# Performance work log

Hardware: AMD Instinct MI355X
Metric: run time of the kernel (lower is better)

Reference implementation:

```python
import jax, jax.numpy as jnp
import numpy as np

N, T, INPUT_DIM, HIDDEN_DIM = 8, 4096, 128, 128


def setup_inputs() -> dict:
    key = jax.random.key(0)
    k_h, k_wq, k_bq, k_wk, k_bk = jax.random.split(key, 5)
    s = 1.0 / np.sqrt(INPUT_DIM)
    return {
        "H": jax.random.normal(k_h, (N, T, INPUT_DIM), dtype=jnp.float32),
        "Wq": jax.random.uniform(k_wq, (INPUT_DIM, HIDDEN_DIM), jnp.float32, -s, s),
        "bq": jax.random.uniform(k_bq, (HIDDEN_DIM,), jnp.float32, -s, s),
        "Wk": jax.random.uniform(k_wk, (INPUT_DIM, HIDDEN_DIM), jnp.float32, -s, s),
        "bk": jax.random.uniform(k_bk, (HIDDEN_DIM,), jnp.float32, -s, s),
    }


def reference(H, Wq, bq, Wk, bk):
    # Q, K: [N, T, hidden]
    Q = jnp.einsum("ntd,dh->nth", H, Wq) + bq
    K = jnp.einsum("ntd,dh->nth", H, Wk) + bk
    # Faithful quirk: original scales by sqrt(K.transpose(-1,-2).size(-1)) == sqrt(T),
    # NOT sqrt(hidden_dim).
    T_ = H.shape[1]
    scale = 1.0 / jnp.sqrt(jnp.asarray(T_, dtype=H.dtype))
    A = jnp.einsum("nth,nsh->nts", Q, K) * scale  # [N, T, T]
    A = jax.nn.softmax(A, axis=-1)
    # Attention applied directly to H (no V projection), plus residual.
    return jnp.einsum("nts,nsd->ntd", A, H) + H
```

## Files before the change

kernel.cpp:

```cpp
#include <hip/hip_runtime.h>
#include <hip/hip_bf16.h>

typedef __attribute__((ext_vector_type(4))) float f32x4;
typedef __attribute__((ext_vector_type(16))) float f32x16;
typedef __attribute__((ext_vector_type(8))) short s16x8;
typedef unsigned int u32;

#define DEVINL static __device__ __forceinline__

constexpr int TDIM = 4096;
constexpr int DDIM = 128;
constexpr float QSCALE = 1.4426950408889634f / 64.0f;

DEVINL unsigned short f2bf(float f) {
  union { float f; unsigned u; } v; v.f = f;
  unsigned r = v.u + 0x7fffu + ((v.u >> 16) & 1u);
  return (unsigned short)(r >> 16);
}

__global__ __launch_bounds__(256) void prep_kernel(
    const float* __restrict__ Wq, const float* __restrict__ Wk,
    const float* __restrict__ bq, unsigned short* __restrict__ Mt,
    float* __restrict__ u) {
  int idx = blockIdx.x * 256 + threadIdx.x;
  int e = idx >> 7, d = idx & 127;
  float acc = 0.f;
#pragma unroll 4
  for (int h = 0; h < 128; ++h) acc += Wq[d * 128 + h] * Wk[e * 128 + h];
  Mt[e * 128 + d] = f2bf(acc);
  if (blockIdx.x == 0 && threadIdx.x < 128) {
    float a = 0.f;
#pragma unroll 4
    for (int h = 0; h < 128; ++h) a += Wk[threadIdx.x * 128 + h] * bq[h];
    u[threadIdx.x] = a;
  }
}

__global__ __launch_bounds__(256) void proj_kernel(
    const float* __restrict__ H, const unsigned short* __restrict__ Mt,
    const float* __restrict__ u, char* __restrict__ Qb,
    char* __restrict__ Kb, char* __restrict__ Vt) {
  __shared__ __align__(16) unsigned short hs[64][136];
  __shared__ __align__(16) char qs[16384];
  __shared__ __align__(16) char kt[16384];
  __shared__ __align__(16) char vt[16384];
  int b = blockIdx.x;
  int n = b >> 6;
  int t0 = (b & 63) << 6;
  int tid = threadIdx.x;
  const float* Hrow = H + (size_t)(n * TDIM + t0) * DDIM;
#pragma unroll
  for (int k = 0; k < 8; ++k) {
    int e = tid + k * 256;
    int r = e >> 5;
    int c = (e & 31) << 2;
    f32x4 v = *(const f32x4*)(Hrow + r * DDIM + c);
    unsigned short bf[4] = {f2bf(v.x), f2bf(v.y), f2bf(v.z), f2bf(v.w)};
    unsigned short* p = &hs[r][c];
    p[0] = bf[0]; p[1] = bf[1]; p[2] = bf[2]; p[3] = bf[3];
    int kbyte = r * 256 + ((c * 2) ^ ((r & 15) << 4));
    unsigned short* kp = (unsigned short*)(kt + kbyte);
    kp[0] = bf[0]; kp[1] = bf[1]; kp[2] = bf[2]; kp[3] = bf[3];
    int p32 = r >> 5, tl = r & 31;
#pragma unroll
    for (int j = 0; j < 4; ++j) {
      int d = c + j;
      int dp = d >> 1, half = d & 1;
      int byte = p32 * 8192 + dp * 128 +
                 ((half * 64 + tl * 2) ^ ((dp & 7) << 4));
      *(unsigned short*)(vt + byte) = bf[j];
    }
  }
  __syncthreads();
  int w = tid >> 6, ln = tid & 63;
  int lm = ln & 15, lg = ln >> 4;
  int m0 = w * 16;
  s16x8 af[4];
#pragma unroll
  for (int kf = 0; kf < 4; ++kf)
    af[kf] = *(const s16x8*)&hs[m0 + lm][kf * 32 + lg * 8];
#pragma unroll
  for (int nt = 0; nt < 8; ++nt) {
    f32x4 acc = {0.f, 0.f, 0.f, 0.f};
#pragma unroll
    for (int kf = 0; kf < 4; ++kf) {
      s16x8 bfr = *(const s16x8*)&Mt[(nt * 16 + lm) * 128 + kf * 32 + lg * 8];
      acc = __builtin_amdgcn_mfma_f32_16x16x32_bf16(af[kf], bfr, acc, 0, 0, 0);
    }
    int e = nt * 16 + lm;
    float bv = u[e];
#pragma unroll
    for (int i = 0; i < 4; ++i) {
      int tl = m0 + lg * 4 + i;
      int byte = tl * 256 + ((e * 2) ^ ((tl & 15) << 4));
      *(unsigned short*)(qs + byte) = f2bf((acc[i] + bv) * QSCALE);
    }
  }
  __syncthreads();
  size_t base = (size_t)(n * TDIM + t0) * 256;
  size_t vbase = (size_t)(n * 128 + (t0 >> 5)) * 8192;
#pragma unroll
  for (int k = 0; k < 4; ++k) {
    int off = tid * 16 + k * 4096;
    *(f32x4*)(Qb + base + off) = *(const f32x4*)(qs + off);
    *(f32x4*)(Kb + base + off) = *(const f32x4*)(kt + off);
    *(f32x4*)(Vt + vbase + off) = *(const f32x4*)(vt + off);
  }
}

DEVINL void stage8(const char* g, char* s, int ln) {
#pragma unroll
  for (int j = 0; j < 8; ++j) {
    __builtin_amdgcn_global_load_lds(
        (const __attribute__((address_space(1))) void*)(g + j * 1024 + ln * 16),
        (__attribute__((address_space(3))) void*)(s + j * 1024), 16, 0, 0);
  }
}

__global__ __launch_bounds__(512, 2) void attn_kernel(
    const char* __restrict__ Qsw, const char* __restrict__ Ksw,
    const char* __restrict__ Vsw, const float* __restrict__ H,
    float* __restrict__ Out) {
  __shared__ __align__(16) char lds[131072];
  int b = blockIdx.x;
  int n = b & 7;
  int q0 = (b >> 3) << 7;
  int tid = threadIdx.x;
  int w = tid >> 6, ln = tid & 63;
  int q32 = ln & 31, hi = ln >> 5;
  int qg = w >> 2;
  int kvs = w & 3;
  int qrow = q0 + qg * 64;
  int swz = (q32 & 15) << 4;
  int dpl = q32 >> 1;
  int vcol = (q32 & 1) * 64;

  const char* Kn = Ksw + (size_t)n * (TDIM * 256);
  const char* Vn = Vsw + (size_t)n * (128 * 8192);

  const char* Qlo = Qsw + (size_t)(n * TDIM + qrow + q32) * 256;
  const char* Qhi = Qlo + 32 * 256;
  s16x8 qfl[8], qfh[8];
#pragma unroll
  for (int d = 0; d < 8; ++d) {
    int off = (d * 32 + hi * 16) ^ swz;
    qfl[d] = *(const s16x8*)(Qlo + off);
    qfh[d] = *(const s16x8*)(Qhi + off);
  }

  f32x16 o[8];
#pragma unroll
  for (int i = 0; i < 8; ++i) o[i] = (f32x16)0.0f;
  float lsl = 0.f, lsh = 0.f;

  int stp = w & 3, typ = w >> 2;
  {
    const char* g = typ ? (Vn + (size_t)(stp * 32) * 8192)
                        : (Kn + (size_t)(stp * 1024) * 256);
    stage8(g, lds + stp * 16384 + typ * 8192, ln);
  }
  __syncthreads();

  for (int it = 0; it < 32; ++it) {
    int c = it & 1;
    if (it < 31) {
      int kvn = stp * 1024 + (it + 1) * 32;
      const char* g = typ ? (Vn + (size_t)(kvn >> 5) * 8192)
                          : (Kn + (size_t)kvn * 256);
      stage8(g, lds + (c ^ 1) * 65536 + stp * 16384 + typ * 8192, ln);
    }
    const char* kb = lds + c * 65536 + kvs * 16384;
    const char* vb = kb + 8192;

    f32x16 sl = (f32x16)0.0f, sh = (f32x16)0.0f;
    __builtin_amdgcn_s_setprio(1);
#pragma unroll
    for (int d = 0; d < 8; ++d) {
      s16x8 ka = *(const s16x8*)(kb + (q32 * 256 + ((d * 32 + hi * 16) ^ swz)));
      sl = __builtin_amdgcn_mfma_f32_32x32x16_bf16(ka, qfl[d], sl, 0, 0, 0);
      sh = __builtin_amdgcn_mfma_f32_32x32x16_bf16(ka, qfh[d], sh, 0, 0, 0);
    }
    __builtin_amdgcn_s_setprio(0);

#pragma unroll
    for (int r = 0; r < 16; ++r) {
      sl[r] = __builtin_amdgcn_exp2f(sl[r]);
      lsl += sl[r];
      sh[r] = __builtin_amdgcn_exp2f(sh[r]);
      lsh += sh[r];
    }

    s16x8 pal[2], pah[2];
    {
      u32 P2[8];
#pragma unroll
      for (int r = 0; r < 8; ++r)
        asm("v_cvt_pk_bf16_f32 %0, %1, %2"
            : "=v"(P2[r]) : "v"(sl[2 * r]), "v"(sl[2 * r + 1]));
#pragma unroll
      for (int b2 = 0; b2 < 2; ++b2) {
        u32 a0 = P2[b2 * 4 + 0], c0 = P2[b2 * 4 + 2];
        u32 a1 = P2[b2 * 4 + 1], c1 = P2[b2 * 4 + 3];
        asm("v_permlane32_swap_b32 %0, %1" : "+v"(a0), "+v"(c0));
        asm("v_permlane32_swap_b32 %0, %1" : "+v"(a1), "+v"(c1));
        union { u32 u[4]; s16x8 v; } pk;
        pk.u[0] = a0; pk.u[1] = a1; pk.u[2] = c0; pk.u[3] = c1;
        pal[b2] = pk.v;
      }
#pragma unroll
      for (int r = 0; r < 8; ++r)
        asm("v_cvt_pk_bf16_f32 %0, %1, %2"
            : "=v"(P2[r]) : "v"(sh[2 * r]), "v"(sh[2 * r + 1]));
#pragma unroll
      for (int b2 = 0; b2 < 2; ++b2) {
        u32 a0 = P2[b2 * 4 + 0], c0 = P2[b2 * 4 + 2];
        u32 a1 = P2[b2 * 4 + 1], c1 = P2[b2 * 4 + 3];
        asm("v_permlane32_swap_b32 %0, %1" : "+v"(a0), "+v"(c0));
        asm("v_permlane32_swap_b32 %0, %1" : "+v"(a1), "+v"(c1));
        union { u32 u[4]; s16x8 v; } pk;
        pk.u[0] = a0; pk.u[1] = a1; pk.u[2] = c0; pk.u[3] = c1;
        pah[b2] = pk.v;
      }
    }

    __builtin_amdgcn_s_setprio(1);
#pragma unroll
    for (int ks = 0; ks < 2; ++ks) {
#pragma unroll
      for (int dt = 0; dt < 4; ++dt) {
        s16x8 vv = *(const s16x8*)(vb + ((dt * 16 + dpl) * 128 +
                        ((vcol + ks * 32 + hi * 16) ^ ((dpl & 7) << 4))));
        o[dt] = __builtin_amdgcn_mfma_f32_32x32x16_bf16(pal[ks], vv, o[dt], 0, 0, 0);
        o[4 + dt] = __builtin_amdgcn_mfma_f32_32x32x16_bf16(pah[ks], vv, o[4 + dt], 0, 0, 0);
      }
    }
    __builtin_amdgcn_s_setprio(0);
    __syncthreads();
  }

#define DUMP_O(dst)                                                      \
  {                                                                      \
    char* _d = (dst);                                                    \
    _Pragma("unroll") for (int i = 0; i < 8; ++i)                        \
      _Pragma("unroll") for (int c4 = 0; c4 < 4; ++c4) {                 \
        f32x4 ch = {o[i][c4 * 4 + 0], o[i][c4 * 4 + 1],                  \
                    o[i][c4 * 4 + 2], o[i][c4 * 4 + 3]};                 \
        *(f32x4*)(_d + ((i * 4 + c4) * 64 + ln) * 16) = ch;              \
      }                                                                  \
  }
#define ADD_O(src)                                                       \
  {                                                                      \
    const char* _s = (src);                                              \
    _Pragma("unroll") for (int i = 0; i < 8; ++i)                        \
      _Pragma("unroll") for (int c4 = 0; c4 < 4; ++c4) {                 \
        f32x4 ch = *(const f32x4*)(_s + ((i * 4 + c4) * 64 + ln) * 16);  \
        o[i][c4 * 4 + 0] += ch.x; o[i][c4 * 4 + 1] += ch.y;              \
        o[i][c4 * 4 + 2] += ch.z; o[i][c4 * 4 + 3] += ch.w;              \
      }                                                                  \
  }
  if (kvs & 1) DUMP_O(lds + (qg * 2 + (kvs >> 1)) * 32768);
  __syncthreads();
  if (!(kvs & 1)) ADD_O(lds + (qg * 2 + (kvs >> 1)) * 32768);
  __syncthreads();
  if (kvs == 2) DUMP_O(lds + qg * 2 * 32768);
  {
    float* lt = (float*)(lds + (qg * 2 + 1) * 32768);
    lt[((kvs * 2 + hi) * 32 + q32) * 2 + 0] = lsl;
    lt[((kvs * 2 + hi) * 32 + q32) * 2 + 1] = lsh;
  }
  __syncthreads();
  if (kvs == 0) {
    ADD_O(lds + qg * 2 * 32768);
    const float* lt = (const float*)(lds + (qg * 2 + 1) * 32768);
    const float* Hn = H + (size_t)n * TDIM * DDIM;
    float* On = Out + (size_t)n * TDIM * DDIM;
#pragma unroll
    for (int r = 0; r < 16; ++r) {
      int qr = (r & 3) + 8 * (r >> 2) + 4 * hi;
      float suml = 0.f, sumh = 0.f;
#pragma unroll
      for (int t8 = 0; t8 < 8; ++t8) {
        suml += lt[(t8 * 32 + qr) * 2 + 0];
        sumh += lt[(t8 * 32 + qr) * 2 + 1];
      }
      float il = 1.0f / suml, ih = 1.0f / sumh;
#pragma unroll
      for (int dt = 0; dt < 4; ++dt) {
        size_t ilo = (size_t)(qrow + qr) * DDIM + dt * 32 + q32;
        size_t ihi = (size_t)(qrow + 32 + qr) * DDIM + dt * 32 + q32;
        On[ilo] = o[dt][r] * il + Hn[ilo];
        On[ihi] = o[4 + dt][r] * ih + Hn[ihi];
      }
    }
  }
#undef DUMP_O
#undef ADD_O
}

extern "C" void kernel_launch(void* const* d_in, const int* in_sizes, int n_in,
                              void* d_out, int out_size, void* d_ws, size_t ws_size,
                              hipStream_t stream) {
  const float* H  = (const float*)d_in[0];
  const float* Wq = (const float*)d_in[1];
  const float* bq = (const float*)d_in[2];
  const float* Wk = (const float*)d_in[3];
  const float* bk = (const float*)d_in[4];
  (void)bk;
  float* Out = (float*)d_out;
  char* ws = (char*)d_ws;
  unsigned short* Mt = (unsigned short*)(ws);
  float* u = (float*)(ws + 32768);
  char* Qb = ws + 65536;
  char* Kb = ws + 65536 + 8388608;
  char* Vt = ws + 65536 + 2 * 8388608;

  prep_kernel<<<64, 256, 0, stream>>>(Wq, Wk, bq, Mt, u);
  proj_kernel<<<512, 256, 0, stream>>>(H, Mt, u, Qb, Kb, Vt);
  attn_kernel<<<256, 512, 0, stream>>>(Qb, Kb, Vt, H, Out);
}
```

Baseline: 117.2 us.

## Split KV across blocks with bf16 partial outputs and separate merge kernel

```diff
diff --git a/kernel.cpp b/kernel.cpp
--- a/kernel.cpp
+++ b/kernel.cpp
@@ -65,9 +65,9 @@
 #pragma unroll
     for (int j = 0; j < 4; ++j) {
       int d = c + j;
-      int dp = d >> 1, half = d & 1;
-      int byte = p32 * 8192 + dp * 128 +
-                 ((half * 64 + tl * 2) ^ ((dp & 7) << 4));
+      int rq = d >> 2;
+      int byte = p32 * 8192 + rq * 256 +
+                 (((d & 3) * 64 + tl * 2) ^ ((rq & 15) << 4));
       *(unsigned short*)(vt + byte) = bf[j];
     }
   }
@@ -117,26 +117,25 @@
   }
 }
 
-__global__ __launch_bounds__(512, 2) void attn_kernel(
+__global__ __launch_bounds__(128, 2) void attn_kernel(
     const char* __restrict__ Qsw, const char* __restrict__ Ksw,
-    const char* __restrict__ Vsw, const float* __restrict__ H,
-    float* __restrict__ Out) {
-  __shared__ __align__(16) char lds[131072];
+    const char* __restrict__ Vsw, u32* __restrict__ OutU,
+    u32* __restrict__ OpU, float* __restrict__ Lp) {
+  __shared__ __align__(16) char kbuf[2][8192];
+  __shared__ __align__(16) char vbuf[2][8192];
   int b = blockIdx.x;
   int n = b & 7;
-  int q0 = (b >> 3) << 7;
+  int st = (b >> 3) & 3;
+  int q0 = (b >> 5) << 7;
   int tid = threadIdx.x;
   int w = tid >> 6, ln = tid & 63;
   int q32 = ln & 31, hi = ln >> 5;
-  int qg = w >> 2;
-  int kvs = w & 3;
-  int qrow = q0 + qg * 64;
+  int qrow = q0 + w * 64;
   int swz = (q32 & 15) << 4;
-  int dpl = q32 >> 1;
-  int vcol = (q32 & 1) * 64;
 
   const char* Kn = Ksw + (size_t)n * (TDIM * 256);
   const char* Vn = Vsw + (size_t)n * (128 * 8192);
+  int kv0 = st * 1024;
 
   const char* Qlo = Qsw + (size_t)(n * TDIM + qrow + q32) * 256;
   const char* Qhi = Qlo + 32 * 256;
@@ -153,24 +152,23 @@
   for (int i = 0; i < 8; ++i) o[i] = (f32x16)0.0f;
   float lsl = 0.f, lsh = 0.f;
 
-  int stp = w & 3, typ = w >> 2;
   {
-    const char* g = typ ? (Vn + (size_t)(stp * 32) * 8192)
-                        : (Kn + (size_t)(stp * 1024) * 256);
-    stage8(g, lds + stp * 16384 + typ * 8192, ln);
+    const char* g = w ? (Vn + (size_t)(kv0 >> 5) * 8192)
+                      : (Kn + (size_t)kv0 * 256);
+    stage8(g, w ? vbuf[0] : kbuf[0], ln);
   }
   __syncthreads();
 
   for (int it = 0; it < 32; ++it) {
     int c = it & 1;
     if (it < 31) {
-      int kvn = stp * 1024 + (it + 1) * 32;
-      const char* g = typ ? (Vn + (size_t)(kvn >> 5) * 8192)
-                          : (Kn + (size_t)kvn * 256);
-      stage8(g, lds + (c ^ 1) * 65536 + stp * 16384 + typ * 8192, ln);
-    }
-    const char* kb = lds + c * 65536 + kvs * 16384;
-    const char* vb = kb + 8192;
+      int kvn = kv0 + (it + 1) * 32;
+      const char* g = w ? (Vn + (size_t)(kvn >> 5) * 8192)
+                        : (Kn + (size_t)kvn * 256);
+      stage8(g, w ? vbuf[c ^ 1] : kbuf[c ^ 1], ln);
+    }
+    const char* kb = kbuf[c];
+    const char* vb = vbuf[c];
 
     f32x16 sl = (f32x16)0.0f, sh = (f32x16)0.0f;
     __builtin_amdgcn_s_setprio(1);
@@ -228,8 +226,9 @@
     for (int ks = 0; ks < 2; ++ks) {
 #pragma unroll
       for (int dt = 0; dt < 4; ++dt) {
-        s16x8 vv = *(const s16x8*)(vb + ((dt * 16 + dpl) * 128 +
-                        ((vcol + ks * 32 + hi * 16) ^ ((dpl & 7) << 4))));
+        int rq = dt * 8 + (q32 >> 2);
+        s16x8 vv = *(const s16x8*)(vb + rq * 256 +
+            (((q32 & 3) * 64 + ks * 32 + hi * 16) ^ ((rq & 15) << 4)));
         o[dt] = __builtin_amdgcn_mfma_f32_32x32x16_bf16(pal[ks], vv, o[dt], 0, 0, 0);
         o[4 + dt] = __builtin_amdgcn_mfma_f32_32x32x16_bf16(pah[ks], vv, o[4 + dt], 0, 0, 0);
       }
@@ -238,63 +237,49 @@
     __syncthreads();
   }
 
-#define DUMP_O(dst)                                                      \
-  {                                                                      \
-    char* _d = (dst);                                                    \
-    _Pragma("unroll") for (int i = 0; i < 8; ++i)                        \
-      _Pragma("unroll") for (int c4 = 0; c4 < 4; ++c4) {                 \
-        f32x4 ch = {o[i][c4 * 4 + 0], o[i][c4 * 4 + 1],                  \
-                    o[i][c4 * 4 + 2], o[i][c4 * 4 + 3]};                 \
-        *(f32x4*)(_d + ((i * 4 + c4) * 64 + ln) * 16) = ch;              \
-      }                                                                  \
-  }
-#define ADD_O(src)                                                       \
-  {                                                                      \
-    const char* _s = (src);                                              \
-    _Pragma("unroll") for (int i = 0; i < 8; ++i)                        \
-      _Pragma("unroll") for (int c4 = 0; c4 < 4; ++c4) {                 \
-        f32x4 ch = *(const f32x4*)(_s + ((i * 4 + c4) * 64 + ln) * 16);  \
-        o[i][c4 * 4 + 0] += ch.x; o[i][c4 * 4 + 1] += ch.y;              \
-        o[i][c4 * 4 + 2] += ch.z; o[i][c4 * 4 + 3] += ch.w;              \
-      }                                                                  \
-  }
-  if (kvs & 1) DUMP_O(lds + (qg * 2 + (kvs >> 1)) * 32768);
-  __syncthreads();
-  if (!(kvs & 1)) ADD_O(lds + (qg * 2 + (kvs >> 1)) * 32768);
-  __syncthreads();
-  if (kvs == 2) DUMP_O(lds + qg * 2 * 32768);
-  {
-    float* lt = (float*)(lds + (qg * 2 + 1) * 32768);
-    lt[((kvs * 2 + hi) * 32 + q32) * 2 + 0] = lsl;
-    lt[((kvs * 2 + hi) * 32 + q32) * 2 + 1] = lsh;
-  }
-  __syncthreads();
-  if (kvs == 0) {
-    ADD_O(lds + qg * 2 * 32768);
-    const float* lt = (const float*)(lds + (qg * 2 + 1) * 32768);
-    const float* Hn = H + (size_t)n * TDIM * DDIM;
-    float* On = Out + (size_t)n * TDIM * DDIM;
-#pragma unroll
-    for (int r = 0; r < 16; ++r) {
-      int qr = (r & 3) + 8 * (r >> 2) + 4 * hi;
-      float suml = 0.f, sumh = 0.f;
-#pragma unroll
-      for (int t8 = 0; t8 < 8; ++t8) {
-        suml += lt[(t8 * 32 + qr) * 2 + 0];
-        sumh += lt[(t8 * 32 + qr) * 2 + 1];
-      }
-      float il = 1.0f / suml, ih = 1.0f / sumh;
-#pragma unroll
-      for (int dt = 0; dt < 4; ++dt) {
-        size_t ilo = (size_t)(qrow + qr) * DDIM + dt * 32 + q32;
-        size_t ihi = (size_t)(qrow + 32 + qr) * DDIM + dt * 32 + q32;
-        On[ilo] = o[dt][r] * il + Hn[ilo];
-        On[ihi] = o[4 + dt][r] * ih + Hn[ihi];
-      }
-    }
-  }
-#undef DUMP_O
-#undef ADD_O
+  u32* Ob = (st < 2 ? OutU : OpU) + (st & 1) * 64;
+#pragma unroll
+  for (int r = 0; r < 16; ++r) {
+    int qr = (r & 3) + 8 * (r >> 2) + 4 * hi;
+    size_t rl = (size_t)(n * TDIM + qrow + qr) * 128;
+    size_t rh = rl + (size_t)32 * 128;
+    u32 a, bb;
+    asm("v_cvt_pk_bf16_f32 %0, %1, %2" : "=v"(a) : "v"(o[0][r]), "v"(o[1][r]));
+    asm("v_cvt_pk_bf16_f32 %0, %1, %2" : "=v"(bb) : "v"(o[2][r]), "v"(o[3][r]));
+    Ob[rl + q32] = a;
+    Ob[rl + 32 + q32] = bb;
+    asm("v_cvt_pk_bf16_f32 %0, %1, %2" : "=v"(a) : "v"(o[4][r]), "v"(o[5][r]));
+    asm("v_cvt_pk_bf16_f32 %0, %1, %2" : "=v"(bb) : "v"(o[6][r]), "v"(o[7][r]));
+    Ob[rh + q32] = a;
+    Ob[rh + 32 + q32] = bb;
+  }
+  Lp[(size_t)(n * TDIM + qrow + q32) * 8 + st * 2 + hi] = lsl;
+  Lp[(size_t)(n * TDIM + qrow + 32 + q32) * 8 + st * 2 + hi] = lsh;
+}
+
+__global__ __launch_bounds__(256) void merge_kernel(
+    u32* __restrict__ OutU, const u32* __restrict__ OpU,
+    const float* __restrict__ Lp, const float* __restrict__ H) {
+  int gid = blockIdx.x * 256 + threadIdx.x;
+  int row = gid >> 6;
+  int pi = gid & 63;
+  int q32 = pi & 31, k = pi >> 5;
+  f32x4 la = *(const f32x4*)(Lp + (size_t)row * 8);
+  f32x4 lb = *(const f32x4*)(Lp + (size_t)row * 8 + 4);
+  float il = 1.0f / (la.x + la.y + la.z + la.w + lb.x + lb.y + lb.z + lb.w);
+  size_t rb = (size_t)row * 128;
+  u32 p0 = OutU[rb + pi], p1 = OutU[rb + 64 + pi];
+  u32 p2 = OpU[rb + pi],  p3 = OpU[rb + 64 + pi];
+#define BL(x) __builtin_bit_cast(float, (u32)((x) << 16))
+#define BH(x) __builtin_bit_cast(float, (u32)((x) & 0xffff0000u))
+  float slo = BL(p0) + BL(p1) + BL(p2) + BL(p3);
+  float shi = BH(p0) + BH(p1) + BH(p2) + BH(p3);
+#undef BL
+#undef BH
+  int d0 = k * 64 + q32, d1 = d0 + 32;
+  float* Outf = (float*)OutU;
+  Outf[rb + d0] = slo * il + H[rb + d0];
+  Outf[rb + d1] = shi * il + H[rb + d1];
 }
 
 extern "C" void kernel_launch(void* const* d_in, const int* in_sizes, int n_in,
@@ -306,15 +291,18 @@
   const float* Wk = (const float*)d_in[3];
   const float* bk = (const float*)d_in[4];
   (void)bk;
-  float* Out = (float*)d_out;
+  u32* OutU = (u32*)d_out;
   char* ws = (char*)d_ws;
   unsigned short* Mt = (unsigned short*)(ws);
   float* u = (float*)(ws + 32768);
   char* Qb = ws + 65536;
-  char* Kb = ws + 65536 + 8388608;
-  char* Vt = ws + 65536 + 2 * 8388608;
+  char* Kb = Qb + 8388608;
+  char* Vt = Kb + 8388608;
+  u32* OpU = (u32*)(Vt + 8388608);
+  float* Lp = (float*)(ws + 65536 + 3 * 8388608 + 16777216);
 
   prep_kernel<<<64, 256, 0, stream>>>(Wq, Wk, bq, Mt, u);
   proj_kernel<<<512, 256, 0, stream>>>(H, Mt, u, Qb, Kb, Vt);
-  attn_kernel<<<256, 512, 0, stream>>>(Qb, Kb, Vt, H, Out);
-}
+  attn_kernel<<<1024, 128, 0, stream>>>(Qb, Kb, Vt, OutU, OpU, Lp);
+  merge_kernel<<<8192, 256, 0, stream>>>(OutU, OpU, Lp, H);
+}
```

Measured after the change: 113.7 us. 3.0% less time.
